# Kernel tuning notes

Hardware: AMD Instinct MI355X
Metric: run time of the kernel (lower is better)

The kernel has to match this reference:

```python
import jax, jax.numpy as jnp
import numpy as np

DIM = 768
NUM_HEADS = 12
HEAD_DIM = DIM // NUM_HEADS
SCALE = HEAD_DIM ** -0.5


def setup_inputs() -> dict:
    key = jax.random.key(0)
    k1, k2, k3, k4, k5 = jax.random.split(key, 5)
    B, N = 2, 2048
    x = jax.random.normal(k1, (B, N, DIM), dtype=jnp.float32)
    # nn.Linear weights stored as [out, in]; we keep them as [in, out] for jnp use.
    Wq = jax.random.normal(k2, (DIM, DIM), dtype=jnp.float32) * (DIM ** -0.5)
    Wkv = jax.random.normal(k3, (DIM, 2 * HEAD_DIM), dtype=jnp.float32) * (DIM ** -0.5)
    Wproj = jax.random.normal(k4, (DIM, DIM), dtype=jnp.float32) * (DIM ** -0.5)
    bproj = jax.random.normal(k5, (DIM,), dtype=jnp.float32) * 0.01
    return {"x": x, "Wq": Wq, "Wkv": Wkv, "Wproj": Wproj, "bproj": bproj, "num_layer": 0}


def reference(x, Wq, Wkv, Wproj, bproj, num_layer):
    B, N, C = x.shape
    H, D = NUM_HEADS, HEAD_DIM
    q = (x @ Wq).reshape(B, N, H, D).transpose(0, 2, 1, 3)        # [B,H,N,D]
    kv = (x @ Wkv).reshape(B, N, 2, D)
    k, v = kv[:, :, 0, :], kv[:, :, 1, :]                          # [B,N,D] shared across heads (MQA)
    attn = jnp.einsum('bhid,bjd->bhij', q, k) * SCALE              # [B,H,N,N]
    attn = jax.nn.softmax(attn, axis=-1)
    out = jnp.einsum('bhij,bjd->bhid', attn, v)                    # [B,H,N,D]
    out = out.transpose(0, 2, 1, 3).reshape(B, N, C)
    return out @ Wproj + bproj
```

## Files before the change

### kernel.cpp

```cpp
#include <hip/hip_runtime.h>

#define BATCH 2
#define SEQ   2048
#define DIMC  768
#define HEADS 12
#define HD    64
#define QSCALE 0.1803368801111204f

typedef short bf16x8 __attribute__((ext_vector_type(8)));
typedef float f32x4  __attribute__((ext_vector_type(4)));
typedef float f32x16 __attribute__((ext_vector_type(16)));

__device__ __forceinline__ unsigned short f2bf(float f) {
    union { float f; unsigned int u; } a; a.f = f;
    unsigned int r = a.u + 0x7fffu + ((a.u >> 16) & 1u);
    return (unsigned short)(r >> 16);
}
__device__ __forceinline__ unsigned int pack2bf(float lo, float hi) {
    union { float f; unsigned int u; } a, b; a.f = lo; b.f = hi;
    return __builtin_amdgcn_perm(b.u + 0x8000u, a.u + 0x8000u, 0x07060302);
}
__device__ __forceinline__ float exp2f_fast(float x) { return __builtin_amdgcn_exp2f(x); }

__device__ __forceinline__ void gload16(const unsigned short* g, unsigned short* l) {
    __builtin_amdgcn_global_load_lds(
        (const __attribute__((address_space(1))) unsigned int*)g,
        (__attribute__((address_space(3))) unsigned int*)l, 16, 0, 0);
}

__global__ void prep(const float* __restrict__ Wq, const float* __restrict__ Wkv,
                     const float* __restrict__ Wproj, const float* __restrict__ x,
                     unsigned short* __restrict__ WqT, unsigned short* __restrict__ WkvT,
                     unsigned short* __restrict__ WprT, unsigned short* __restrict__ xb)
{
    const int bid = blockIdx.x, t = threadIdx.x;
    if (bid >= 1248) {
        const size_t base = (size_t)(bid - 1248) * 2048 + (size_t)t * 8;
        float4 v0 = *(const float4*)&x[base];
        float4 v1 = *(const float4*)&x[base + 4];
        uint4 o = { pack2bf(v0.x, v0.y), pack2bf(v0.z, v0.w),
                    pack2bf(v1.x, v1.y), pack2bf(v1.z, v1.w) };
        *(uint4*)&xb[base] = o;
        return;
    }
    __shared__ float sT[32][33];
    const float* W; unsigned short* WT; int N, tb;
    if (bid < 576)      { W = Wq;    WT = WqT;  N = DIMC;   tb = bid; }
    else if (bid < 672) { W = Wkv;   WT = WkvT; N = 2 * HD; tb = bid - 576; }
    else                { W = Wproj; WT = WprT; N = DIMC;   tb = bid - 672; }
    const int tilesN = N / 32;
    const int k0 = (tb / tilesN) * 32, n0 = (tb - (tb / tilesN) * tilesN) * 32;
    const int r = t >> 3, c4 = (t & 7) * 4;
    float4 v = *(const float4*)&W[(size_t)(k0 + r) * N + n0 + c4];
    sT[c4 + 0][r] = v.x; sT[c4 + 1][r] = v.y; sT[c4 + 2][r] = v.z; sT[c4 + 3][r] = v.w;
    __syncthreads();
    ushort4 o = { f2bf(sT[r][c4]), f2bf(sT[r][c4 + 1]), f2bf(sT[r][c4 + 2]), f2bf(sT[r][c4 + 3]) };
    *(ushort4*)&WT[(size_t)(n0 + r) * 768 + k0 + c4] = o;
}

template <int MODE>
__global__ __launch_bounds__(256)
void gemm128(const unsigned short* __restrict__ A, const unsigned short* __restrict__ BT,
             const float* __restrict__ bias, void* __restrict__ C0,
             unsigned short* __restrict__ Kout, unsigned short* __restrict__ VTout)
{
    __shared__ __align__(16) unsigned short sA[2][128 * 128];
    __shared__ __align__(16) unsigned short sB[2][128 * 128];
    const int t = threadIdx.x, lane = t & 63, w = t >> 6;
    const int bm = blockIdx.y * 128, bn = blockIdx.x * 128;
    const int wm = (w >> 1) * 64, wn = (w & 1) * 64;

    const unsigned short* Apt = &A [(size_t)(bm + (lane >> 2)) * DIMC + (lane & 3) * 8];
    const unsigned short* Bpt = &BT[(size_t)(bn + (lane >> 2)) * DIMC + (lane & 3) * 8];

    auto stage = [&](int kt, int bf) {
        const int off = kt * 128;
        #pragma unroll
        for (int kc = 0; kc < 4; ++kc) {
            #pragma unroll
            for (int g = 0; g < 2; ++g) {
                const int rg = 2 * w + g;
                const size_t goff = (size_t)rg * 16 * DIMC + off + kc * 32;
                gload16(Apt + goff, &sA[bf][kc * 4096 + rg * 512]);
                gload16(Bpt + goff, &sB[bf][kc * 4096 + rg * 512]);
            }
        }
    };

    const int fr = lane & 15, fk = (lane >> 4) * 8;

    f32x4 acc[4][4] = {};

    stage(0, 0);
    __syncthreads();
    for (int kt = 0; kt < DIMC / 128; ++kt) {
        const int buf = kt & 1;
        if (kt + 1 < DIMC / 128) stage(kt + 1, buf ^ 1);
        #pragma unroll
        for (int kc = 0; kc < 4; ++kc) {
            bf16x8 af[4], bq[4];
            #pragma unroll
            for (int i = 0; i < 4; ++i)
                af[i] = *(const bf16x8*)&sA[buf][kc * 4096 + (wm + i * 16 + fr) * 32 + fk];
            #pragma unroll
            for (int j = 0; j < 4; ++j)
                bq[j] = *(const bf16x8*)&sB[buf][kc * 4096 + (wn + j * 16 + fr) * 32 + fk];
            #pragma unroll
            for (int i = 0; i < 4; ++i)
                #pragma unroll
                for (int j = 0; j < 4; ++j)
                    acc[i][j] = __builtin_amdgcn_mfma_f32_16x16x32_bf16(af[i], bq[j], acc[i][j], 0, 0, 0);
        }
        __syncthreads();
    }

    const int cn = lane & 15, cm = (lane >> 4) * 4;
    #pragma unroll
    for (int j = 0; j < 4; ++j) {
        const int n = bn + wn + j * 16 + cn;
        #pragma unroll
        for (int i = 0; i < 4; ++i) {
            #pragma unroll
            for (int r = 0; r < 4; ++r) {
                const int m = bm + wm + i * 16 + cm + r;
                float val = acc[i][j][r];
                if (MODE == 0) {
                    if (n < DIMC) {
                        ((unsigned short*)C0)[(size_t)m * DIMC + n] = f2bf(val * QSCALE);
                    } else {
                        const int c2 = n - DIMC;
                        if (c2 < HD) Kout[(size_t)m * HD + c2] = f2bf(val);
                        else {
                            const int bbk = m >> 11, tok = m & (SEQ - 1);
                            VTout[(size_t)bbk * HD * SEQ + (size_t)(c2 - HD) * SEQ + tok] = f2bf(val);
                        }
                    }
                } else {
                    ((float*)C0)[(size_t)m * DIMC + n] = val + bias[n];
                }
            }
        }
    }
}

__global__ __launch_bounds__(256)
void flash_kernel(const unsigned short* __restrict__ Qw, const unsigned short* __restrict__ Kw,
                  const unsigned short* __restrict__ VTw, unsigned short* __restrict__ Ob)
{
    const int qblk = blockIdx.x, h = blockIdx.y, b = blockIdx.z;
    const int tid = threadIdx.x, w = tid >> 6, lane = tid & 63;
    const int l31 = lane & 31, hi = lane >> 5;
    const int kr = w >> 1, qc = w & 1;

    __shared__ __align__(16) unsigned short sK [2][64][72];
    __shared__ __align__(16) unsigned short sVT[2][64][72];
    __shared__ float sL[4][32];
    __shared__ float sLi[2][32];

    const size_t qrow = (size_t)(b * SEQ + qblk * 64 + qc * 32 + l31);
    bf16x8 qf[4];
    #pragma unroll
    for (int s = 0; s < 4; ++s)
        qf[s] = *(const bf16x8*)&Qw[qrow * DIMC + h * HD + s * 16 + hi * 8];

    f32x16 oacc0 = {}, oacc1 = {};
    float lsum = 0.0f;

    const int r_st = tid >> 2, c_st = (tid & 3) * 16;
    const unsigned short* Kp  = &Kw[(size_t)(b * SEQ + r_st) * HD + c_st];
    const unsigned short* VTp = &VTw[(size_t)b * HD * SEQ + (size_t)r_st * SEQ + c_st];

    bf16x8 kg0, kg1, vg0, vg1;
    auto loadKV = [&](int ti) {
        const unsigned short* ks = Kp + (size_t)ti * 64 * HD;
        const unsigned short* vs = VTp + ti * 64;
        kg0 = *(const bf16x8*)&ks[0]; kg1 = *(const bf16x8*)&ks[8];
        vg0 = *(const bf16x8*)&vs[0]; vg1 = *(const bf16x8*)&vs[8];
    };
    auto writeKV = [&](int bf) {
        *(bf16x8*)&sK[bf][r_st][c_st]      = kg0;
        *(bf16x8*)&sK[bf][r_st][c_st + 8]  = kg1;
        *(bf16x8*)&sVT[bf][r_st][c_st]     = vg0;
        *(bf16x8*)&sVT[bf][r_st][c_st + 8] = vg1;
    };

    loadKV(0); writeKV(0); loadKV(1);
    __syncthreads();

    for (int kt = 0; kt < SEQ / 64; ++kt) {
        const int buf = kt & 1;
        if (kt + 1 < SEQ / 64) {
            writeKV(buf ^ 1);
            loadKV(kt + 2 < SEQ / 64 ? kt + 2 : SEQ / 64 - 1);
        }

        f32x16 st = {};
        #pragma unroll
        for (int s = 0; s < 4; ++s) {
            bf16x8 ka = *(const bf16x8*)&sK[buf][kr * 32 + l31][s * 16 + hi * 8];
            st = __builtin_amdgcn_mfma_f32_32x32x16_bf16(ka, qf[s], st, 0, 0, 0);
        }

        uint2 pg[4];
        #pragma unroll
        for (int g = 0; g < 4; ++g) {
            float p0 = exp2f_fast(st[g * 4 + 0]);
            float p1 = exp2f_fast(st[g * 4 + 1]);
            float p2 = exp2f_fast(st[g * 4 + 2]);
            float p3 = exp2f_fast(st[g * 4 + 3]);
            lsum += (p0 + p1) + (p2 + p3);
            pg[g].x = pack2bf(p0, p1);
            pg[g].y = pack2bf(p2, p3);
        }

        #pragma unroll
        for (int s = 0; s < 2; ++s) {
            uint2 send; send.x = hi ? pg[2 * s].x : pg[2 * s + 1].x;
                        send.y = hi ? pg[2 * s].y : pg[2 * s + 1].y;
            uint2 recv; recv.x = __shfl_xor((int)send.x, 32);
                        recv.y = __shfl_xor((int)send.y, 32);
            union { uint4 u4; bf16x8 v; } pa;
            pa.u4.x = hi ? recv.x : pg[2 * s].x;
            pa.u4.y = hi ? recv.y : pg[2 * s].y;
            pa.u4.z = hi ? pg[2 * s + 1].x : recv.x;
            pa.u4.w = hi ? pg[2 * s + 1].y : recv.y;
            bf16x8 vb0 = *(const bf16x8*)&sVT[buf][l31][kr * 32 + s * 16 + hi * 8];
            bf16x8 vb1 = *(const bf16x8*)&sVT[buf][32 + l31][kr * 32 + s * 16 + hi * 8];
            oacc0 = __builtin_amdgcn_mfma_f32_32x32x16_bf16(pa.v, vb0, oacc0, 0, 0, 0);
            oacc1 = __builtin_amdgcn_mfma_f32_32x32x16_bf16(pa.v, vb1, oacc1, 0, 0, 0);
        }
        __syncthreads();
    }

    lsum += __shfl_xor(lsum, 32);
    if (lane < 32) sL[w][l31] = lsum;

    float* scratch = (float*)&sK[0][0][0];
    {
        int rid = qc * 2 + (1 - kr);
        float* rg = scratch + rid * 1024;
        f32x16 give = kr ? oacc0 : oacc1;
        #pragma unroll
        for (int r = 0; r < 16; ++r) rg[r * 64 + lane] = give[r];
    }
    __syncthreads();

    f32x16 own = kr ? oacc1 : oacc0;
    {
        const float* rg = scratch + (qc * 2 + kr) * 1024;
        #pragma unroll
        for (int r = 0; r < 16; ++r) own[r] += rg[r * 64 + lane];
    }
    if (kr == 0 && lane < 32)
        sLi[qc][l31] = 1.0f / (sL[qc][l31] + sL[qc + 2][l31]);
    __syncthreads();

    #pragma unroll
    for (int r = 0; r < 16; ++r) {
        int rq = (r & 3) + 8 * (r >> 2) + 4 * hi;
        float iv = sLi[qc][rq];
        size_t row = (size_t)(b * SEQ + qblk * 64 + qc * 32 + rq);
        Ob[row * DIMC + h * HD + kr * 32 + l31] = f2bf(own[r] * iv);
    }
}

extern "C" void kernel_launch(void* const* d_in, const int* in_sizes, int n_in,
                              void* d_out, int out_size, void* d_ws, size_t ws_size,
                              hipStream_t stream)
{
    const float* x     = (const float*)d_in[0];
    const float* Wq    = (const float*)d_in[1];
    const float* Wkv   = (const float*)d_in[2];
    const float* Wproj = (const float*)d_in[3];
    const float* bproj = (const float*)d_in[4];

    const int M = BATCH * SEQ;
    unsigned short* WqT  = (unsigned short*)d_ws;
    unsigned short* WkvT = WqT  + DIMC * DIMC;
    unsigned short* WprT = WkvT + 2 * HD * DIMC;
    unsigned short* Qw   = WprT + DIMC * DIMC;
    unsigned short* Kw   = Qw   + (size_t)M * DIMC;
    unsigned short* VTw  = Kw   + (size_t)M * HD;
    unsigned short* Ob   = VTw  + (size_t)BATCH * HD * SEQ;
    unsigned short* xb   = Ob;

    prep<<<1248 + 1536, 256, 0, stream>>>(Wq, Wkv, Wproj, x, WqT, WkvT, WprT, xb);
    gemm128<0><<<dim3(7, M / 128), 256, 0, stream>>>(xb, WqT, nullptr, Qw, Kw, VTw);
    flash_kernel<<<dim3(SEQ / 64, HEADS, BATCH), 256, 0, stream>>>(Qw, Kw, VTw, Ob);
    gemm128<1><<<dim3(6, M / 128), 256, 0, stream>>>(Ob, WprT, bproj, d_out, nullptr, nullptr);
}
```

Measured before the change: 156.1 us.

## Give each wave full key tiles over 32 queries, doubling query block size

The flash kernel now gives each of the 4 waves its own 32 query rows and has it process the whole 64-key tile. Each block therefore covers 128 queries instead of 64, so K/V tiles staged in shared memory are reused across twice as many queries. This removes the split-K partial output exchange and reduction through shared memory at the end. It also adds s_setprio around the MFMA sections. The grid halves to 384 blocks and register pressure rises from two score accumulators per wave, which may reduce occupancy.

After: 164.8 us. 5.6% more time.

```diff
diff --git a/kernel.cpp b/kernel.cpp
--- a/kernel.cpp
+++ b/kernel.cpp
@@ -150,14 +150,12 @@
     const int qblk = blockIdx.x, h = blockIdx.y, b = blockIdx.z;
     const int tid = threadIdx.x, w = tid >> 6, lane = tid & 63;
     const int l31 = lane & 31, hi = lane >> 5;
-    const int kr = w >> 1, qc = w & 1;
 
     __shared__ __align__(16) unsigned short sK [2][64][72];
     __shared__ __align__(16) unsigned short sVT[2][64][72];
-    __shared__ float sL[4][32];
-    __shared__ float sLi[2][32];
-
-    const size_t qrow = (size_t)(b * SEQ + qblk * 64 + qc * 32 + l31);
+    __shared__ float sLi[4][32];
+
+    const size_t qrow = (size_t)(b * SEQ + qblk * 128 + w * 32 + l31);
     bf16x8 qf[4];
     #pragma unroll
     for (int s = 0; s < 4; ++s)
@@ -194,73 +192,74 @@
             loadKV(kt + 2 < SEQ / 64 ? kt + 2 : SEQ / 64 - 1);
         }
 
-        f32x16 st = {};
+        f32x16 st0 = {}, st1 = {};
+        __builtin_amdgcn_s_setprio(1);
         #pragma unroll
         for (int s = 0; s < 4; ++s) {
-            bf16x8 ka = *(const bf16x8*)&sK[buf][kr * 32 + l31][s * 16 + hi * 8];
-            st = __builtin_amdgcn_mfma_f32_32x32x16_bf16(ka, qf[s], st, 0, 0, 0);
-        }
-
-        uint2 pg[4];
+            bf16x8 ka0 = *(const bf16x8*)&sK[buf][l31][s * 16 + hi * 8];
+            bf16x8 ka1 = *(const bf16x8*)&sK[buf][32 + l31][s * 16 + hi * 8];
+            st0 = __builtin_amdgcn_mfma_f32_32x32x16_bf16(ka0, qf[s], st0, 0, 0, 0);
+            st1 = __builtin_amdgcn_mfma_f32_32x32x16_bf16(ka1, qf[s], st1, 0, 0, 0);
+        }
+        __builtin_amdgcn_s_setprio(0);
+
+        uint2 pg0[4], pg1[4];
+        float ls0 = 0.0f, ls1 = 0.0f;
         #pragma unroll
         for (int g = 0; g < 4; ++g) {
-            float p0 = exp2f_fast(st[g * 4 + 0]);
-            float p1 = exp2f_fast(st[g * 4 + 1]);
-            float p2 = exp2f_fast(st[g * 4 + 2]);
-            float p3 = exp2f_fast(st[g * 4 + 3]);
-            lsum += (p0 + p1) + (p2 + p3);
-            pg[g].x = pack2bf(p0, p1);
-            pg[g].y = pack2bf(p2, p3);
-        }
-
-        #pragma unroll
-        for (int s = 0; s < 2; ++s) {
-            uint2 send; send.x = hi ? pg[2 * s].x : pg[2 * s + 1].x;
-                        send.y = hi ? pg[2 * s].y : pg[2 * s + 1].y;
-            uint2 recv; recv.x = __shfl_xor((int)send.x, 32);
-                        recv.y = __shfl_xor((int)send.y, 32);
-            union { uint4 u4; bf16x8 v; } pa;
-            pa.u4.x = hi ? recv.x : pg[2 * s].x;
-            pa.u4.y = hi ? recv.y : pg[2 * s].y;
-            pa.u4.z = hi ? pg[2 * s + 1].x : recv.x;
-            pa.u4.w = hi ? pg[2 * s + 1].y : recv.y;
-            bf16x8 vb0 = *(const bf16x8*)&sVT[buf][l31][kr * 32 + s * 16 + hi * 8];
-            bf16x8 vb1 = *(const bf16x8*)&sVT[buf][32 + l31][kr * 32 + s * 16 + hi * 8];
-            oacc0 = __builtin_amdgcn_mfma_f32_32x32x16_bf16(pa.v, vb0, oacc0, 0, 0, 0);
-            oacc1 = __builtin_amdgcn_mfma_f32_32x32x16_bf16(pa.v, vb1, oacc1, 0, 0, 0);
-        }
+            float a0 = exp2f_fast(st0[g * 4 + 0]);
+            float a1 = exp2f_fast(st0[g * 4 + 1]);
+            float a2 = exp2f_fast(st0[g * 4 + 2]);
+            float a3 = exp2f_fast(st0[g * 4 + 3]);
+            ls0 += (a0 + a1) + (a2 + a3);
+            pg0[g].x = pack2bf(a0, a1);
+            pg0[g].y = pack2bf(a2, a3);
+            float b0 = exp2f_fast(st1[g * 4 + 0]);
+            float b1 = exp2f_fast(st1[g * 4 + 1]);
+            float b2 = exp2f_fast(st1[g * 4 + 2]);
+            float b3 = exp2f_fast(st1[g * 4 + 3]);
+            ls1 += (b0 + b1) + (b2 + b3);
+            pg1[g].x = pack2bf(b0, b1);
+            pg1[g].y = pack2bf(b2, b3);
+        }
+        lsum += ls0 + ls1;
+
+        auto pv = [&](const uint2 (&pgk)[4], int kh) {
+            #pragma unroll
+            for (int s = 0; s < 2; ++s) {
+                uint2 send; send.x = hi ? pgk[2 * s].x : pgk[2 * s + 1].x;
+                            send.y = hi ? pgk[2 * s].y : pgk[2 * s + 1].y;
+                uint2 recv; recv.x = __shfl_xor((int)send.x, 32);
+                            recv.y = __shfl_xor((int)send.y, 32);
+                union { uint4 u4; bf16x8 v; } pa;
+                pa.u4.x = hi ? recv.x : pgk[2 * s].x;
+                pa.u4.y = hi ? recv.y : pgk[2 * s].y;
+                pa.u4.z = hi ? pgk[2 * s + 1].x : recv.x;
+                pa.u4.w = hi ? pgk[2 * s + 1].y : recv.y;
+                bf16x8 vb0 = *(const bf16x8*)&sVT[buf][l31][kh * 32 + s * 16 + hi * 8];
+                bf16x8 vb1 = *(const bf16x8*)&sVT[buf][32 + l31][kh * 32 + s * 16 + hi * 8];
+                __builtin_amdgcn_s_setprio(1);
+                oacc0 = __builtin_amdgcn_mfma_f32_32x32x16_bf16(pa.v, vb0, oacc0, 0, 0, 0);
+                oacc1 = __builtin_amdgcn_mfma_f32_32x32x16_bf16(pa.v, vb1, oacc1, 0, 0, 0);
+                __builtin_amdgcn_s_setprio(0);
+            }
+        };
+        pv(pg0, 0);
+        pv(pg1, 1);
         __syncthreads();
     }
 
     lsum += __shfl_xor(lsum, 32);
-    if (lane < 32) sL[w][l31] = lsum;
-
-    float* scratch = (float*)&sK[0][0][0];
-    {
-        int rid = qc * 2 + (1 - kr);
-        float* rg = scratch + rid * 1024;
-        f32x16 give = kr ? oacc0 : oacc1;
-        #pragma unroll
-        for (int r = 0; r < 16; ++r) rg[r * 64 + lane] = give[r];
-    }
-    __syncthreads();
-
-    f32x16 own = kr ? oacc1 : oacc0;
-    {
-        const float* rg = scratch + (qc * 2 + kr) * 1024;
-        #pragma unroll
-        for (int r = 0; r < 16; ++r) own[r] += rg[r * 64 + lane];
-    }
-    if (kr == 0 && lane < 32)
-        sLi[qc][l31] = 1.0f / (sL[qc][l31] + sL[qc + 2][l31]);
+    if (lane < 32) sLi[w][l31] = 1.0f / lsum;
     __syncthreads();
 
     #pragma unroll
     for (int r = 0; r < 16; ++r) {
         int rq = (r & 3) + 8 * (r >> 2) + 4 * hi;
-        float iv = sLi[qc][rq];
-        size_t row = (size_t)(b * SEQ + qblk * 64 + qc * 32 + rq);
-        Ob[row * DIMC + h * HD + kr * 32 + l31] = f2bf(own[r] * iv);
+        float iv = sLi[w][rq];
+        size_t row = (size_t)(b * SEQ + qblk * 128 + w * 32 + rq);
+        Ob[row * DIMC + h * HD + l31]      = f2bf(oacc0[r] * iv);
+        Ob[row * DIMC + h * HD + 32 + l31] = f2bf(oacc1[r] * iv);
     }
 }
 
@@ -286,6 +285,6 @@
 
     prep<<<1248 + 1536, 256, 0, stream>>>(Wq, Wkv, Wproj, x, WqT, WkvT, WprT, xb);
     gemm128<0><<<dim3(7, M / 128), 256, 0, stream>>>(xb, WqT, nullptr, Qw, Kw, VTw);
-    flash_kernel<<<dim3(SEQ / 64, HEADS, BATCH), 256, 0, stream>>>(Qw, Kw, VTw, Ob);
+    flash_kernel<<<dim3(SEQ / 128, HEADS, BATCH), 256, 0, stream>>>(Qw, Kw, VTw, Ob);
     gemm128<1><<<dim3(6, M / 128), 256, 0, stream>>>(Ob, WprT, bproj, d_out, nullptr, nullptr);
 }
```
